# Kernel optimization log

Measured on AMD Instinct MI355X. Metric: run time of the kernel, lower is better.

## Reference

```python
import jax, jax.numpy as jnp
import numpy as np

B, P, M, C = 128, 8732, 16, 3
THRESHOLD, NEG_POS_RATIO, ALPHA = 0.5, 3, 1.0


def xy_to_cxcy(xy):
    return jnp.concatenate([(xy[..., 2:] + xy[..., :2]) / 2.0, xy[..., 2:] - xy[..., :2]], axis=-1)


def cxcy_to_xy(cxcy):
    return jnp.concatenate([cxcy[..., :2] - cxcy[..., 2:] / 2.0, cxcy[..., :2] + cxcy[..., 2:] / 2.0], axis=-1)


def cxcy_to_gcxgcy(cxcy, priors_cxcy):
    return jnp.concatenate([
        (cxcy[..., :2] - priors_cxcy[..., :2]) / (priors_cxcy[..., 2:] / 10.0),
        jnp.log(cxcy[..., 2:] / priors_cxcy[..., 2:]) * 5.0], axis=-1)


def jaccard(a, b):
    # a: (M,4) xyxy, b: (P,4) xyxy -> (M,P) IoU
    lt = jnp.maximum(a[:, None, :2], b[None, :, :2])
    rb = jnp.minimum(a[:, None, 2:], b[None, :, 2:])
    wh = jnp.clip(rb - lt, 0.0)
    inter = wh[..., 0] * wh[..., 1]
    area_a = (a[:, 2] - a[:, 0]) * (a[:, 3] - a[:, 1])
    area_b = (b[:, 2] - b[:, 0]) * (b[:, 3] - b[:, 1])
    return inter / (area_a[:, None] + area_b[None, :] - inter)


def setup_inputs() -> dict:
    key = jax.random.key(0)
    k1, k2, k3, k4, k5, k6 = jax.random.split(key, 6)
    predicted_locs = jax.random.normal(k1, (B, P, 4), dtype=jnp.float32)
    predicted_scores = jax.random.normal(k2, (B, P, C), dtype=jnp.float32)
    xy = jax.random.uniform(k3, (B, M, 2), minval=0.0, maxval=0.7)
    wh = jax.random.uniform(k4, (B, M, 2), minval=0.05, maxval=0.3)
    boxes = jnp.concatenate([xy, xy + wh], axis=-1).astype(jnp.float32)
    labels = jax.random.randint(k5, (B, M), 1, 4)  # classes {1,2,3}
    pc = jax.random.uniform(k6, (P, 2), minval=0.0, maxval=1.0)
    pwh = jax.random.uniform(jax.random.fold_in(k6, 1), (P, 2), minval=0.05, maxval=0.5)
    priors_cxcy = jnp.concatenate([pc, pwh], axis=-1).astype(jnp.float32)
    return {"predicted_locs": predicted_locs, "predicted_scores": predicted_scores,
            "boxes": boxes, "labels": labels, "priors_cxcy": priors_cxcy}


def _match_one(boxes_i, labels_i, priors_xy, priors_cxcy):
    ov = jaccard(boxes_i, priors_xy)                # (M, P)
    ov_prior = ov.max(axis=0)                       # best overlap per prior
    obj_prior = ov.argmax(axis=0)                   # best object per prior
    prior_obj = ov.argmax(axis=1)                   # best prior per object
    n_obj = boxes_i.shape[0]
    obj_prior = obj_prior.at[prior_obj].set(jnp.arange(n_obj))
    ov_prior = ov_prior.at[prior_obj].set(1.0)
    lab = jnp.where(ov_prior < THRESHOLD, 0, labels_i[obj_prior])
    tl = cxcy_to_gcxgcy(xy_to_cxcy(boxes_i[obj_prior]), priors_cxcy)
    return tl, lab


def reference(predicted_locs, predicted_scores, boxes, labels, priors_cxcy):
    priors_xy = cxcy_to_xy(priors_cxcy)
    true_locs, true_classes = jax.vmap(_match_one, in_axes=(0, 0, None, None))(
        boxes, labels, priors_xy, priors_cxcy)      # (B,P,4), (B,P)
    positive = true_classes > 0                      # (B,P)
    n_pos = positive.sum(axis=1)                     # (B,)
    n_pos_total = n_pos.sum()

    # localization loss: L1Loss (mean over selected positive elements)
    l1 = jnp.abs(predicted_locs - true_locs).sum(axis=-1)   # (B,P)
    loc_loss = jnp.where(n_pos_total > 0,
                         (l1 * positive).sum() / (4.0 * jnp.maximum(n_pos_total, 1).astype(jnp.float32)),
                         0.0)

    # multi-label one-hot targets (classes 1,2,3; 3 = pair -> targets cols 1&2)
    tc = true_classes.reshape(-1)
    ignore = tc == -1
    pair = tc == 3
    target = jax.nn.one_hot(tc + 1, 5, dtype=predicted_scores.dtype)[:, 1:4]  # (B*P,3)
    target = target.at[:, 1].set(jnp.where(pair, 1.0, target[:, 1]))
    target = target.at[:, 2].set(jnp.where(pair, 1.0, target[:, 2]))

    # BCEWithLogits, summed over classes
    logits = predicted_scores.reshape(-1, C)
    bce = (jnp.logaddexp(0.0, logits) - logits * target).sum(axis=1)  # (B*P,)
    conf_all = jnp.where(ignore, 0.0, bce).reshape(true_classes.shape)  # (B,P)

    conf_pos = (conf_all * positive).sum()
    conf_neg = jnp.where(positive, 0.0, conf_all)
    conf_neg_sorted = -jnp.sort(-conf_neg, axis=1)   # descending per row
    ranks = jnp.arange(P)[None, :]
    hard_neg = ranks < (NEG_POS_RATIO * n_pos)[:, None]
    conf_hard_neg = (conf_neg_sorted * hard_neg).sum()

    conf_loss = (conf_hard_neg + conf_pos) / (1e-10 + n_pos_total.astype(jnp.float32))
    total = conf_loss + ALPHA * loc_loss
    return total, conf_loss, loc_loss, n_pos
```

## Files before the change

kernel.cpp:

```cpp
#include <hip/hip_runtime.h>
#include <hip/hip_fp16.h>
#include <cstdint>
#include <cmath>

#define B_ 128
#define P_ 8732
#define QU_ 2183
#define M_ 16
#define NT 1024
#define NW 16
#define NP9 9

__device__ __forceinline__ float softplusf(float x) {
    float e = __builtin_amdgcn_exp2f(fabsf(x) * -1.44269504f);
    return fmaxf(x, 0.0f) + 0.69314718f * __builtin_amdgcn_logf(1.0f + e);
}

__device__ __forceinline__ float wred_sum_f(float v) {
#pragma unroll
    for (int o = 32; o > 0; o >>= 1) v += __shfl_down(v, o, 64);
    return v;
}
__device__ __forceinline__ int wred_sum_i(int v) {
#pragma unroll
    for (int o = 32; o > 0; o >>= 1) v += __shfl_down(v, o, 64);
    return v;
}

__global__ __launch_bounds__(NT) void mbox_match_kernel(
    const float* __restrict__ plocs,
    const float* __restrict__ pscores,
    const float* __restrict__ boxes,
    const int*   __restrict__ labels,
    const float* __restrict__ priors,
    unsigned char* __restrict__ objov,
    unsigned short* __restrict__ bcew,
    int2* __restrict__ cand,
    float* __restrict__ pcf, float* __restrict__ plc, int* __restrict__ pnp,
    unsigned int* __restrict__ gz)
{
    __shared__ unsigned long long s_ovp[QU_];
    __shared__ float s_boxes[M_ * 4];
    __shared__ float s_area[M_];
    __shared__ int   s_labels[M_];
    __shared__ float s_pf[2 * NW];
    __shared__ int   s_pi[NW];

    const int bk = blockIdx.x;
    const int r  = bk >> 2;
    const int q  = bk & 3;
    const int tid = threadIdx.x;
    const int lane = tid & 63;
    const int wid = tid >> 6;

    if (bk == 0 && tid < 4) gz[tid] = 0u;

    if (tid < M_ * 4) s_boxes[tid] = boxes[r * M_ * 4 + tid];
    if (tid >= 64 && tid < 64 + M_) s_labels[tid - 64] = labels[r * M_ + (tid - 64)];
    for (int i = tid; i < QU_; i += NT) s_ovp[i] = 15ull;
    __syncthreads();
    if (tid < M_) {
        float x0 = s_boxes[tid*4+0], y0 = s_boxes[tid*4+1];
        float x1 = s_boxes[tid*4+2], y1 = s_boxes[tid*4+3];
        s_area[tid] = (x1 - x0) * (y1 - y0);
    }
    __syncthreads();

    const int p0 = q * QU_;

    {
        const int m = wid;
        const float bx0 = s_boxes[m*4+0], by0 = s_boxes[m*4+1];
        const float bx1 = s_boxes[m*4+2], by1 = s_boxes[m*4+3];
        const float marea = s_area[m];
        const unsigned long long tag = (unsigned long long)(15 - m);
        float bv = -1.0f; int bi = 0x7FFFFFFF;
        for (int p = p0 + lane; p < p0 + QU_; p += 64) {
            float4 pr = ((const float4*)priors)[p];
            float px0 = pr.x - pr.z * 0.5f;
            float py0 = pr.y - pr.w * 0.5f;
            float px1 = pr.x + pr.z * 0.5f;
            float py1 = pr.y + pr.w * 0.5f;
            float ltx = fmaxf(bx0, px0);
            float lty = fmaxf(by0, py0);
            float rbx = fminf(bx1, px1);
            float rby = fminf(by1, py1);
            float wx = fmaxf(rbx - ltx, 0.0f);
            float wy = fmaxf(rby - lty, 0.0f);
            float inter = wx * wy;
            float ov = inter * __builtin_amdgcn_rcpf(marea + pr.z * pr.w - inter);
            if (ov > 0.0f) {
                unsigned long long pk =
                    ((unsigned long long)__float_as_uint(ov) << 4) | tag;
                atomicMax(&s_ovp[p - p0], pk);
            }
            if (ov > bv) { bv = ov; bi = p; }
        }
#pragma unroll
        for (int o = 32; o > 0; o >>= 1) {
            float v2 = __shfl_down(bv, o, 64);
            int   i2 = __shfl_down(bi, o, 64);
            if (v2 > bv || (v2 == bv && i2 < bi)) { bv = v2; bi = i2; }
        }
        if (lane == 0) cand[bk * M_ + m] = make_int2(__float_as_int(bv), bi);
    }
    __syncthreads();

    int np = 0; float cp = 0.0f, ls = 0.0f;
    for (int p = p0 + tid; p < p0 + QU_; p += NT) {
        unsigned long long u = s_ovp[p - p0];
        int   besti = 15 - (int)(u & 15ull);
        float bestv = __uint_as_float((unsigned int)(u >> 4));
        bool pos = bestv >= 0.5f;
        objov[(size_t)r * P_ + p] = (unsigned char)(besti | (pos ? 0x80 : 0));

        const float* sc = pscores + ((size_t)r * P_ + p) * 3;
        float x0 = sc[0], x1 = sc[1], x2 = sc[2];
        int lab = pos ? s_labels[besti] : 0;
        float t0 = (lab == 0) ? 1.0f : 0.0f;
        float t1 = (lab == 1 || lab == 3) ? 1.0f : 0.0f;
        float t2 = (lab == 2 || lab == 3) ? 1.0f : 0.0f;
        float bce = (softplusf(x0) - x0*t0) + (softplusf(x1) - x1*t1) + (softplusf(x2) - x2*t2);
        float hb = 0.0f;
        if (pos) {
            np++; cp += bce;
            float4 pr = ((const float4*)priors)[p];
            float bx0 = s_boxes[besti*4+0], by0 = s_boxes[besti*4+1];
            float bx1 = s_boxes[besti*4+2], by1 = s_boxes[besti*4+3];
            float cx = (bx0 + bx1) * 0.5f, cy = (by0 + by1) * 0.5f;
            float w = bx1 - bx0, hh = by1 - by0;
            float g0 = (cx - pr.x) / (pr.z * 0.1f);
            float g1 = (cy - pr.y) / (pr.w * 0.1f);
            float g2 = logf(w / pr.z) * 5.0f;
            float g3 = logf(hh / pr.w) * 5.0f;
            float4 pl = ((const float4*)plocs)[(size_t)r * P_ + p];
            ls += fabsf(pl.x - g0) + fabsf(pl.y - g1) + fabsf(pl.z - g2) + fabsf(pl.w - g3);
        } else {
            hb = bce;
        }
        bcew[(size_t)r * P_ + p] = __half_as_ushort(__float2half(hb));
    }

    {
        float cpr = wred_sum_f(cp);
        float lsr = wred_sum_f(ls);
        int   npr = wred_sum_i(np);
        if (lane == 0) { s_pf[wid] = cpr; s_pf[NW + wid] = lsr; s_pi[wid] = npr; }
    }
    __syncthreads();
    if (tid == 0) {
        float c2 = 0.0f, l2 = 0.0f; int n2 = 0;
#pragma unroll
        for (int w = 0; w < NW; ++w) { c2 += s_pf[w]; l2 += s_pf[NW + w]; n2 += s_pi[w]; }
        pcf[bk] = c2; plc[bk] = l2; pnp[bk] = n2;
    }
}

__global__ __launch_bounds__(NT) void mbox_loss_kernel(
    const float* __restrict__ plocs,
    const float* __restrict__ pscores,
    const float* __restrict__ boxes,
    const int*   __restrict__ labels,
    const float* __restrict__ priors,
    const unsigned char* __restrict__ objov,
    const unsigned short* __restrict__ bcew,
    const int2* __restrict__ cand,
    const float* __restrict__ pcf, const float* __restrict__ plc,
    const int* __restrict__ pnp,
    float* __restrict__ out,
    unsigned int* __restrict__ g_cnt,
    float* __restrict__ g_conf, float* __restrict__ g_loc, int* __restrict__ g_np)
{
    __shared__ float s_boxes[M_ * 4];
    __shared__ int   s_labels[M_];
    __shared__ int   s_po[M_];
    __shared__ float s_pf[2 * NW];
    __shared__ int   s_pi[NW];
    __shared__ int   s_cnt2[2][NW];
    __shared__ float s_scal[2];
    __shared__ int   s_npos;

    const int r = blockIdx.x;
    const int tid = threadIdx.x;
    const int lane = tid & 63;
    const int wid = tid >> 6;

    if (tid < M_ * 4) s_boxes[tid] = boxes[r * M_ * 4 + tid];
    if (tid >= 64 && tid < 64 + M_) s_labels[tid - 64] = labels[r * M_ + (tid - 64)];
    if (tid >= 128 && tid < 128 + M_) {
        int m = tid - 128;
        int2 c = cand[(r * 4) * M_ + m];
        float v = __int_as_float(c.x); int idx = c.y;
#pragma unroll
        for (int qq = 1; qq < 4; ++qq) {
            int2 c2 = cand[(r * 4 + qq) * M_ + m];
            float v2 = __int_as_float(c2.x);
            if (v2 > v) { v = v2; idx = c2.y; }
        }
        s_po[m] = idx;
    }
    __syncthreads();

    int fv_b[NP9];
#pragma unroll
    for (int i = 0; i < NP9; ++i) {
        int p = tid + i * NT;
        fv_b[i] = (p < P_) ? (int)bcew[(size_t)r * P_ + p] : 0;
    }

    if (wid == 0) {
        float dcp = 0.0f, dls = 0.0f; int dnp = 0;
        if (lane < M_) {
            const int m = lane;
            const int idx = s_po[m];
            bool owner = true;
            for (int m2 = m + 1; m2 < M_; ++m2)
                if (s_po[m2] == idx) owner = false;
            if (owner) {
                unsigned char byte = objov[(size_t)r * P_ + idx];
                bool oldpos = (byte & 0x80) != 0;
                int  oldobj = byte & 15;
                const float* sc = pscores + ((size_t)r * P_ + idx) * 3;
                float x0 = sc[0], x1 = sc[1], x2 = sc[2];
                float S = softplusf(x0) + softplusf(x1) + softplusf(x2);
                float4 pr = ((const float4*)priors)[idx];
                float4 pl = ((const float4*)plocs)[(size_t)r * P_ + idx];
                {
                    int lab = s_labels[m];
                    float t0 = (lab == 0) ? 1.0f : 0.0f;
                    float t1 = (lab == 1 || lab == 3) ? 1.0f : 0.0f;
                    float t2 = (lab == 2 || lab == 3) ? 1.0f : 0.0f;
                    dcp += S - (x0*t0 + x1*t1 + x2*t2);
                    float bx0 = s_boxes[m*4+0], by0 = s_boxes[m*4+1];
                    float bx1 = s_boxes[m*4+2], by1 = s_boxes[m*4+3];
                    float cx = (bx0+bx1)*0.5f, cy = (by0+by1)*0.5f;
                    float w = bx1-bx0, hh = by1-by0;
                    float g0 = (cx - pr.x) / (pr.z * 0.1f);
                    float g1 = (cy - pr.y) / (pr.w * 0.1f);
                    float g2 = logf(w / pr.z) * 5.0f;
                    float g3 = logf(hh / pr.w) * 5.0f;
                    dls += fabsf(pl.x-g0)+fabsf(pl.y-g1)+fabsf(pl.z-g2)+fabsf(pl.w-g3);
                    dnp += 1;
                }
                if (oldpos) {
                    int lab = s_labels[oldobj];
                    float t0 = (lab == 0) ? 1.0f : 0.0f;
                    float t1 = (lab == 1 || lab == 3) ? 1.0f : 0.0f;
                    float t2 = (lab == 2 || lab == 3) ? 1.0f : 0.0f;
                    dcp -= S - (x0*t0 + x1*t1 + x2*t2);
                    float bx0 = s_boxes[oldobj*4+0], by0 = s_boxes[oldobj*4+1];
                    float bx1 = s_boxes[oldobj*4+2], by1 = s_boxes[oldobj*4+3];
                    float cx = (bx0+bx1)*0.5f, cy = (by0+by1)*0.5f;
                    float w = bx1-bx0, hh = by1-by0;
                    float g0 = (cx - pr.x) / (pr.z * 0.1f);
                    float g1 = (cy - pr.y) / (pr.w * 0.1f);
                    float g2 = logf(w / pr.z) * 5.0f;
                    float g3 = logf(hh / pr.w) * 5.0f;
                    dls -= fabsf(pl.x-g0)+fabsf(pl.y-g1)+fabsf(pl.z-g2)+fabsf(pl.w-g3);
                    dnp -= 1;
                }
            }
        }
        dcp = wred_sum_f(dcp);
        dls = wred_sum_f(dls);
        dnp = wred_sum_i(dnp);
        if (lane == 0) {
            float cp = dcp, lsx = dls; int np = dnp;
#pragma unroll
            for (int qq = 0; qq < 4; ++qq) {
                cp  += pcf[r * 4 + qq];
                lsx += plc[r * 4 + qq];
                np  += pnp[r * 4 + qq];
            }
            s_scal[0] = cp; s_scal[1] = lsx; s_npos = np;
        }
    }
    __syncthreads();
    const int npos_row = s_npos;

#pragma unroll
    for (int i = 0; i < NP9; ++i) {
        int p = tid + i * NT;
#pragma unroll
        for (int j = 0; j < M_; ++j)
            if (s_po[j] == p) fv_b[i] = 0;
    }

    int k = 3 * npos_row;
    if (k > P_) k = P_;
    float hard_sum = 0.0f;
    if (k > 0) {
        int lo = -1, hi = 0x7C00;
        for (int it = 0; it < 15; ++it) {
            int mid = (lo + hi) >> 1;
            int c = 0;
#pragma unroll
            for (int i = 0; i < NP9; ++i) c += (fv_b[i] > mid) ? 1 : 0;
            c = wred_sum_i(c);
            if (lane == 0) s_cnt2[it & 1][wid] = c;
            __syncthreads();
            int cnt = 0;
#pragma unroll
            for (int w = 0; w < NW; ++w) cnt += s_cnt2[it & 1][w];
            if (cnt < k) hi = mid; else lo = mid;
        }
        int tb = hi;
        float tval = __half2float(__ushort_as_half((unsigned short)tb));
        float lsum = 0.0f; int lcnt = 0;
#pragma unroll
        for (int i = 0; i < NP9; ++i) {
            if (fv_b[i] > tb) {
                lsum += __half2float(__ushort_as_half((unsigned short)fv_b[i]));
                lcnt++;
            }
        }
        lsum = wred_sum_f(lsum);
        lcnt = wred_sum_i(lcnt);
        if (lane == 0) { s_pf[wid] = lsum; s_pi[wid] = lcnt; }
        __syncthreads();
        if (tid == 0) {
            float sv = 0.0f; int sc2 = 0;
#pragma unroll
            for (int w = 0; w < NW; ++w) { sv += s_pf[w]; sc2 += s_pi[w]; }
            hard_sum = sv + (float)(k - sc2) * tval;
        }
    }

    if (tid == 0) {
        float conf_row = s_scal[0] + hard_sum;
        float loc_row  = s_scal[1];
        out[3 + r] = (float)npos_row;
        atomicAdd(g_conf, conf_row);
        atomicAdd(g_loc,  loc_row);
        atomicAdd(g_np,   npos_row);
        __threadfence();
        unsigned int done = atomicAdd(g_cnt, 1u);
        if (done == B_ - 1) {
            float ct = atomicAdd(g_conf, 0.0f);
            float lt = atomicAdd(g_loc,  0.0f);
            int   np = atomicAdd(g_np,   0);
            float npt = (float)np;
            float conf_loss = ct / (1e-10f + npt);
            float loc_loss = (np > 0) ? lt / (4.0f * fmaxf(npt, 1.0f)) : 0.0f;
            out[0] = conf_loss + loc_loss;
            out[1] = conf_loss;
            out[2] = loc_loss;
        }
    }
}

extern "C" void kernel_launch(void* const* d_in, const int* in_sizes, int n_in,
                              void* d_out, int out_size, void* d_ws, size_t ws_size,
                              hipStream_t stream) {
    const float* plocs   = (const float*)d_in[0];
    const float* pscores = (const float*)d_in[1];
    const float* boxes   = (const float*)d_in[2];
    const int*   labels  = (const int*)  d_in[3];
    const float* priors  = (const float*)d_in[4];
    float* out = (float*)d_out;

    char* ws = (char*)d_ws;
    unsigned int* g_cnt  = (unsigned int*)ws;
    float*        g_conf = (float*)(ws + 4);
    float*        g_loc  = (float*)(ws + 8);
    int*          g_np   = (int*)(ws + 12);
    float*        pcf    = (float*)(ws + 64);
    float*        plc    = (float*)(ws + 2112);
    int*          pnp    = (int*)(ws + 4160);
    int2*         cand   = (int2*)(ws + 8192);
    unsigned char* objov = (unsigned char*)(ws + 73728);
    unsigned short* bcew = (unsigned short*)(ws + 73728 + (size_t)B_ * P_);

    mbox_match_kernel<<<4 * B_, NT, 0, stream>>>(plocs, pscores, boxes, labels, priors,
                                                 objov, bcew, cand, pcf, plc, pnp,
                                                 (unsigned int*)ws);
    mbox_loss_kernel<<<B_, NT, 0, stream>>>(plocs, pscores, boxes, labels, priors,
                                            objov, bcew, cand, pcf, plc, pnp,
                                            out, g_cnt, g_conf, g_loc, g_np);
}
```

Before: 120.6 us.

## Fuse match and loss kernels using per-row last-block completion counter

Merges the two launches into one kernel. Each of the four quarter-row blocks bumps a per-row atomic counter, and the last block to finish runs the hard-negative selection and final reduction. The per-row BCE values are staged in shared memory, reusing the overlap buffer, instead of registers. Positive priors are zeroed with a direct scatter rather than a 16-way compare per element. This removes a launch gap and the global synchronisation between stages, but adds a memset, fence overhead, and a serial tail that runs on only one block per row.

```diff
diff --git a/kernel.cpp b/kernel.cpp
--- a/kernel.cpp
+++ b/kernel.cpp
@@ -27,7 +27,7 @@
     return v;
 }
 
-__global__ __launch_bounds__(NT) void mbox_match_kernel(
+__global__ __launch_bounds__(NT) void mbox_fused_kernel(
     const float* __restrict__ plocs,
     const float* __restrict__ pscores,
     const float* __restrict__ boxes,
@@ -37,7 +37,10 @@
     unsigned short* __restrict__ bcew,
     int2* __restrict__ cand,
     float* __restrict__ pcf, float* __restrict__ plc, int* __restrict__ pnp,
-    unsigned int* __restrict__ gz)
+    unsigned int* __restrict__ row_cnt,
+    float* __restrict__ out,
+    unsigned int* __restrict__ g_cnt,
+    float* __restrict__ g_conf, float* __restrict__ g_loc, int* __restrict__ g_np)
 {
     __shared__ unsigned long long s_ovp[QU_];
     __shared__ float s_boxes[M_ * 4];
@@ -45,6 +48,13 @@
     __shared__ int   s_labels[M_];
     __shared__ float s_pf[2 * NW];
     __shared__ int   s_pi[NW];
+    __shared__ int   s_po[M_];
+    __shared__ int   s_cnt2[2][NW];
+    __shared__ float s_scal[2];
+    __shared__ int   s_npos;
+    __shared__ int   s_islast;
+
+    unsigned short* s_fv = (unsigned short*)s_ovp;
 
     const int bk = blockIdx.x;
     const int r  = bk >> 2;
@@ -52,8 +62,6 @@
     const int tid = threadIdx.x;
     const int lane = tid & 63;
     const int wid = tid >> 6;
-
-    if (bk == 0 && tid < 4) gz[tid] = 0u;
 
     if (tid < M_ * 4) s_boxes[tid] = boxes[r * M_ * 4 + tid];
     if (tid >= 64 && tid < 64 + M_) s_labels[tid - 64] = labels[r * M_ + (tid - 64)];
@@ -153,60 +161,36 @@
 #pragma unroll
         for (int w = 0; w < NW; ++w) { c2 += s_pf[w]; l2 += s_pf[NW + w]; n2 += s_pi[w]; }
         pcf[bk] = c2; plc[bk] = l2; pnp[bk] = n2;
-    }
-}
-
-__global__ __launch_bounds__(NT) void mbox_loss_kernel(
-    const float* __restrict__ plocs,
-    const float* __restrict__ pscores,
-    const float* __restrict__ boxes,
-    const int*   __restrict__ labels,
-    const float* __restrict__ priors,
-    const unsigned char* __restrict__ objov,
-    const unsigned short* __restrict__ bcew,
-    const int2* __restrict__ cand,
-    const float* __restrict__ pcf, const float* __restrict__ plc,
-    const int* __restrict__ pnp,
-    float* __restrict__ out,
-    unsigned int* __restrict__ g_cnt,
-    float* __restrict__ g_conf, float* __restrict__ g_loc, int* __restrict__ g_np)
-{
-    __shared__ float s_boxes[M_ * 4];
-    __shared__ int   s_labels[M_];
-    __shared__ int   s_po[M_];
-    __shared__ float s_pf[2 * NW];
-    __shared__ int   s_pi[NW];
-    __shared__ int   s_cnt2[2][NW];
-    __shared__ float s_scal[2];
-    __shared__ int   s_npos;
-
-    const int r = blockIdx.x;
-    const int tid = threadIdx.x;
-    const int lane = tid & 63;
-    const int wid = tid >> 6;
-
-    if (tid < M_ * 4) s_boxes[tid] = boxes[r * M_ * 4 + tid];
-    if (tid >= 64 && tid < 64 + M_) s_labels[tid - 64] = labels[r * M_ + (tid - 64)];
-    if (tid >= 128 && tid < 128 + M_) {
-        int m = tid - 128;
-        int2 c = cand[(r * 4) * M_ + m];
+        __builtin_amdgcn_fence(__ATOMIC_RELEASE, "agent");
+        unsigned int prev = atomicAdd(&row_cnt[r], 1u);
+        if (prev == 3u) {
+            __builtin_amdgcn_fence(__ATOMIC_ACQUIRE, "agent");
+            s_islast = 1;
+        } else {
+            s_islast = 0;
+        }
+    }
+    __syncthreads();
+    if (!s_islast) return;
+
+
+    if (tid < M_) {
+        int2 c = cand[(r * 4) * M_ + tid];
         float v = __int_as_float(c.x); int idx = c.y;
 #pragma unroll
         for (int qq = 1; qq < 4; ++qq) {
-            int2 c2 = cand[(r * 4 + qq) * M_ + m];
+            int2 c2 = cand[(r * 4 + qq) * M_ + tid];
             float v2 = __int_as_float(c2.x);
             if (v2 > v) { v = v2; idx = c2.y; }
         }
-        s_po[m] = idx;
-    }
-    __syncthreads();
-
-    int fv_b[NP9];
+        s_po[tid] = idx;
+    }
 #pragma unroll
     for (int i = 0; i < NP9; ++i) {
         int p = tid + i * NT;
-        fv_b[i] = (p < P_) ? (int)bcew[(size_t)r * P_ + p] : 0;
-    }
+        if (p < P_) s_fv[p] = bcew[(size_t)r * P_ + p];
+    }
+    __syncthreads();
 
     if (wid == 0) {
         float dcp = 0.0f, dls = 0.0f; int dnp = 0;
@@ -265,26 +249,19 @@
         dls = wred_sum_f(dls);
         dnp = wred_sum_i(dnp);
         if (lane == 0) {
-            float cp = dcp, lsx = dls; int np = dnp;
+            float cp2 = dcp, lsx = dls; int np2 = dnp;
 #pragma unroll
             for (int qq = 0; qq < 4; ++qq) {
-                cp  += pcf[r * 4 + qq];
+                cp2 += pcf[r * 4 + qq];
                 lsx += plc[r * 4 + qq];
-                np  += pnp[r * 4 + qq];
-            }
-            s_scal[0] = cp; s_scal[1] = lsx; s_npos = np;
-        }
-    }
+                np2 += pnp[r * 4 + qq];
+            }
+            s_scal[0] = cp2; s_scal[1] = lsx; s_npos = np2;
+        }
+    }
+    if (wid == 1 && lane < M_) s_fv[s_po[lane]] = 0;
     __syncthreads();
     const int npos_row = s_npos;
-
-#pragma unroll
-    for (int i = 0; i < NP9; ++i) {
-        int p = tid + i * NT;
-#pragma unroll
-        for (int j = 0; j < M_; ++j)
-            if (s_po[j] == p) fv_b[i] = 0;
-    }
 
     int k = 3 * npos_row;
     if (k > P_) k = P_;
@@ -295,7 +272,10 @@
             int mid = (lo + hi) >> 1;
             int c = 0;
 #pragma unroll
-            for (int i = 0; i < NP9; ++i) c += (fv_b[i] > mid) ? 1 : 0;
+            for (int i = 0; i < NP9; ++i) {
+                int p = tid + i * NT;
+                if (p < P_) c += ((int)s_fv[p] > mid) ? 1 : 0;
+            }
             c = wred_sum_i(c);
             if (lane == 0) s_cnt2[it & 1][wid] = c;
             __syncthreads();
@@ -309,9 +289,13 @@
         float lsum = 0.0f; int lcnt = 0;
 #pragma unroll
         for (int i = 0; i < NP9; ++i) {
-            if (fv_b[i] > tb) {
-                lsum += __half2float(__ushort_as_half((unsigned short)fv_b[i]));
-                lcnt++;
+            int p = tid + i * NT;
+            if (p < P_) {
+                int fv = (int)s_fv[p];
+                if (fv > tb) {
+                    lsum += __half2float(__ushort_as_half((unsigned short)fv));
+                    lcnt++;
+                }
             }
         }
         lsum = wred_sum_f(lsum);
@@ -338,10 +322,10 @@
         if (done == B_ - 1) {
             float ct = atomicAdd(g_conf, 0.0f);
             float lt = atomicAdd(g_loc,  0.0f);
-            int   np = atomicAdd(g_np,   0);
-            float npt = (float)np;
+            int   np2 = atomicAdd(g_np,   0);
+            float npt = (float)np2;
             float conf_loss = ct / (1e-10f + npt);
-            float loc_loss = (np > 0) ? lt / (4.0f * fmaxf(npt, 1.0f)) : 0.0f;
+            float loc_loss = (np2 > 0) ? lt / (4.0f * fmaxf(npt, 1.0f)) : 0.0f;
             out[0] = conf_loss + loc_loss;
             out[1] = conf_loss;
             out[2] = loc_loss;
@@ -360,21 +344,22 @@
     float* out = (float*)d_out;
 
     char* ws = (char*)d_ws;
-    unsigned int* g_cnt  = (unsigned int*)ws;
-    float*        g_conf = (float*)(ws + 4);
-    float*        g_loc  = (float*)(ws + 8);
-    int*          g_np   = (int*)(ws + 12);
-    float*        pcf    = (float*)(ws + 64);
-    float*        plc    = (float*)(ws + 2112);
-    int*          pnp    = (int*)(ws + 4160);
-    int2*         cand   = (int2*)(ws + 8192);
-    unsigned char* objov = (unsigned char*)(ws + 73728);
-    unsigned short* bcew = (unsigned short*)(ws + 73728 + (size_t)B_ * P_);
-
-    mbox_match_kernel<<<4 * B_, NT, 0, stream>>>(plocs, pscores, boxes, labels, priors,
-                                                 objov, bcew, cand, pcf, plc, pnp,
-                                                 (unsigned int*)ws);
-    mbox_loss_kernel<<<B_, NT, 0, stream>>>(plocs, pscores, boxes, labels, priors,
-                                            objov, bcew, cand, pcf, plc, pnp,
-                                            out, g_cnt, g_conf, g_loc, g_np);
-}
+    unsigned int* g_cnt   = (unsigned int*)ws;
+    float*        g_conf  = (float*)(ws + 4);
+    float*        g_loc   = (float*)(ws + 8);
+    int*          g_np    = (int*)(ws + 12);
+    unsigned int* row_cnt = (unsigned int*)(ws + 16);
+    float*        pcf     = (float*)(ws + 576);
+    float*        plc     = (float*)(ws + 2624);
+    int*          pnp     = (int*)(ws + 4672);
+    int2*         cand    = (int2*)(ws + 8192);
+    unsigned char* objov  = (unsigned char*)(ws + 73728);
+    unsigned short* bcew  = (unsigned short*)(ws + 73728 + (size_t)B_ * P_);
+
+    hipMemsetAsync(ws, 0, 528, stream);
+
+    mbox_fused_kernel<<<4 * B_, NT, 0, stream>>>(
+        plocs, pscores, boxes, labels, priors,
+        objov, bcew, cand, pcf, plc, pnp, row_cnt,
+        out, g_cnt, g_conf, g_loc, g_np);
+}
```

New measurement: 134.2 us. +11.3%, slower.

## Assign priors to threads and loop over objects, dropping shared-memory atomic max

Applied to the files above, without the earlier changes.

The match kernel now gives each thread up to three priors and loops over all 16 boxes in registers, in place of one wavefront per box doing 64-bit atomicMax into a shared per-prior array. Best object per prior is kept in registers. Best prior per object is found with a wave shuffle reduction per box, then a cross-wave reduction in shared memory. Prior and score loads are issued at kernel start so they overlap the box setup. Tie-breaking on equal overlaps follows the in-register max rather than the packed atomic tag, so the index chosen may differ from before.

```diff
diff --git a/kernel.cpp b/kernel.cpp
--- a/kernel.cpp
+++ b/kernel.cpp
@@ -10,6 +10,7 @@
 #define NT 1024
 #define NW 16
 #define NP9 9
+#define TAIL_ (QU_ - 2*NT)
 
 __device__ __forceinline__ float softplusf(float x) {
     float e = __builtin_amdgcn_exp2f(fabsf(x) * -1.44269504f);
@@ -25,6 +26,39 @@
 #pragma unroll
     for (int o = 32; o > 0; o >>= 1) v += __shfl_down(v, o, 64);
     return v;
+}
+
+__device__ __forceinline__ void phaseD(
+    int r, int p, float bv, int bm, float4 pr,
+    float x0, float x1, float x2,
+    const float* s_boxes, const int* s_labels,
+    const float* __restrict__ plocs,
+    unsigned char* __restrict__ objov, unsigned short* __restrict__ bcew,
+    int& np, float& cp, float& ls)
+{
+    bool pos = bv >= 0.5f;
+    objov[(size_t)r * P_ + p] = (unsigned char)(bm | (pos ? 0x80 : 0));
+    int lab = pos ? s_labels[bm] : 0;
+    float t0 = (lab == 0) ? 1.0f : 0.0f;
+    float t1 = (lab == 1 || lab == 3) ? 1.0f : 0.0f;
+    float t2 = (lab == 2 || lab == 3) ? 1.0f : 0.0f;
+    float bce = (softplusf(x0) - x0*t0) + (softplusf(x1) - x1*t1) + (softplusf(x2) - x2*t2);
+    float hb = 0.0f;
+    if (pos) {
+        np++; cp += bce;
+        float4 bb = ((const float4*)s_boxes)[bm];
+        float cx = (bb.x + bb.z) * 0.5f, cy = (bb.y + bb.w) * 0.5f;
+        float w = bb.z - bb.x, hh = bb.w - bb.y;
+        float g0 = (cx - pr.x) / (pr.z * 0.1f);
+        float g1 = (cy - pr.y) / (pr.w * 0.1f);
+        float g2 = logf(w / pr.z) * 5.0f;
+        float g3 = logf(hh / pr.w) * 5.0f;
+        float4 pl = ((const float4*)plocs)[(size_t)r * P_ + p];
+        ls += fabsf(pl.x - g0) + fabsf(pl.y - g1) + fabsf(pl.z - g2) + fabsf(pl.w - g3);
+    } else {
+        hb = bce;
+    }
+    bcew[(size_t)r * P_ + p] = __half_as_ushort(__float2half(hb));
 }
 
 __global__ __launch_bounds__(NT) void mbox_match_kernel(
@@ -39,10 +73,10 @@
     float* __restrict__ pcf, float* __restrict__ plc, int* __restrict__ pnp,
     unsigned int* __restrict__ gz)
 {
-    __shared__ unsigned long long s_ovp[QU_];
     __shared__ float s_boxes[M_ * 4];
     __shared__ float s_area[M_];
     __shared__ int   s_labels[M_];
+    __shared__ int2  s_cand[NW][M_];
     __shared__ float s_pf[2 * NW];
     __shared__ int   s_pi[NW];
 
@@ -52,12 +86,28 @@
     const int tid = threadIdx.x;
     const int lane = tid & 63;
     const int wid = tid >> 6;
+    const int p0 = q * QU_;
 
     if (bk == 0 && tid < 4) gz[tid] = 0u;
+
+    const int  pA = p0 + tid;
+    const int  pB = p0 + NT + tid;
+    const bool cok = tid < TAIL_;
+    const int  pC = cok ? (p0 + 2 * NT + tid) : pA;
+
+    float4 prA = ((const float4*)priors)[pA];
+    float4 prB = ((const float4*)priors)[pB];
+    float4 prC = ((const float4*)priors)[pC];
+
+    const float* scA = pscores + ((size_t)r * P_ + pA) * 3;
+    const float* scB = pscores + ((size_t)r * P_ + pB) * 3;
+    const float* scC = pscores + ((size_t)r * P_ + pC) * 3;
+    float xA0 = scA[0], xA1 = scA[1], xA2 = scA[2];
+    float xB0 = scB[0], xB1 = scB[1], xB2 = scB[2];
+    float xC0 = scC[0], xC1 = scC[1], xC2 = scC[2];
 
     if (tid < M_ * 4) s_boxes[tid] = boxes[r * M_ * 4 + tid];
     if (tid >= 64 && tid < 64 + M_) s_labels[tid - 64] = labels[r * M_ + (tid - 64)];
-    for (int i = tid; i < QU_; i += NT) s_ovp[i] = 15ull;
     __syncthreads();
     if (tid < M_) {
         float x0 = s_boxes[tid*4+0], y0 = s_boxes[tid*4+1];
@@ -66,88 +116,89 @@
     }
     __syncthreads();
 
-    const int p0 = q * QU_;
-
-    {
-        const int m = wid;
-        const float bx0 = s_boxes[m*4+0], by0 = s_boxes[m*4+1];
-        const float bx1 = s_boxes[m*4+2], by1 = s_boxes[m*4+3];
-        const float marea = s_area[m];
-        const unsigned long long tag = (unsigned long long)(15 - m);
-        float bv = -1.0f; int bi = 0x7FFFFFFF;
-        for (int p = p0 + lane; p < p0 + QU_; p += 64) {
-            float4 pr = ((const float4*)priors)[p];
-            float px0 = pr.x - pr.z * 0.5f;
-            float py0 = pr.y - pr.w * 0.5f;
-            float px1 = pr.x + pr.z * 0.5f;
-            float py1 = pr.y + pr.w * 0.5f;
-            float ltx = fmaxf(bx0, px0);
-            float lty = fmaxf(by0, py0);
-            float rbx = fminf(bx1, px1);
-            float rby = fminf(by1, py1);
-            float wx = fmaxf(rbx - ltx, 0.0f);
-            float wy = fmaxf(rby - lty, 0.0f);
-            float inter = wx * wy;
-            float ov = inter * __builtin_amdgcn_rcpf(marea + pr.z * pr.w - inter);
-            if (ov > 0.0f) {
-                unsigned long long pk =
-                    ((unsigned long long)__float_as_uint(ov) << 4) | tag;
-                atomicMax(&s_ovp[p - p0], pk);
-            }
-            if (ov > bv) { bv = ov; bi = p; }
-        }
+    float aX0 = prA.x - prA.z*0.5f, aY0 = prA.y - prA.w*0.5f;
+    float aX1 = prA.x + prA.z*0.5f, aY1 = prA.y + prA.w*0.5f;
+    float aAr = prA.z * prA.w;
+    float bX0 = prB.x - prB.z*0.5f, bY0 = prB.y - prB.w*0.5f;
+    float bX1 = prB.x + prB.z*0.5f, bY1 = prB.y + prB.w*0.5f;
+    float bAr = prB.z * prB.w;
+    float cX0 = prC.x - prC.z*0.5f, cY0 = prC.y - prC.w*0.5f;
+    float cX1 = prC.x + prC.z*0.5f, cY1 = prC.y + prC.w*0.5f;
+    float cAr = prC.z * prC.w;
+
+    float bvA = -1.0f, bvB = -1.0f, bvC = -1.0f;
+    int   bmA = 0,     bmB = 0,     bmC = 0;
+
+#pragma unroll
+    for (int m = 0; m < M_; ++m) {
+        float4 bb = ((const float4*)s_boxes)[m];
+        float mar = s_area[m];
+
+        float ltx, lty, rbx, rby, wx, wy, inter;
+
+        ltx = fmaxf(bb.x, aX0); lty = fmaxf(bb.y, aY0);
+        rbx = fminf(bb.z, aX1); rby = fminf(bb.w, aY1);
+        wx = fmaxf(rbx - ltx, 0.0f); wy = fmaxf(rby - lty, 0.0f);
+        inter = wx * wy;
+        float ovA = inter * __builtin_amdgcn_rcpf(mar + aAr - inter);
+
+        ltx = fmaxf(bb.x, bX0); lty = fmaxf(bb.y, bY0);
+        rbx = fminf(bb.z, bX1); rby = fminf(bb.w, bY1);
+        wx = fmaxf(rbx - ltx, 0.0f); wy = fmaxf(rby - lty, 0.0f);
+        inter = wx * wy;
+        float ovB = inter * __builtin_amdgcn_rcpf(mar + bAr - inter);
+
+        ltx = fmaxf(bb.x, cX0); lty = fmaxf(bb.y, cY0);
+        rbx = fminf(bb.z, cX1); rby = fminf(bb.w, cY1);
+        wx = fmaxf(rbx - ltx, 0.0f); wy = fmaxf(rby - lty, 0.0f);
+        inter = wx * wy;
+        float ovC = inter * __builtin_amdgcn_rcpf(mar + cAr - inter);
+        ovC = cok ? ovC : -1.0f;
+
+        if (ovA > bvA) { bvA = ovA; bmA = m; }
+        if (ovB > bvB) { bvB = ovB; bmB = m; }
+        if (ovC > bvC) { bvC = ovC; bmC = m; }
+
+        float v = ovA; int which = 0;
+        if (ovB > v) { v = ovB; which = 1; }
+        if (ovC > v) { v = ovC; which = 2; }
+        int idx = p0 + tid + (which << 10);
+
 #pragma unroll
         for (int o = 32; o > 0; o >>= 1) {
-            float v2 = __shfl_down(bv, o, 64);
-            int   i2 = __shfl_down(bi, o, 64);
-            if (v2 > bv || (v2 == bv && i2 < bi)) { bv = v2; bi = i2; }
-        }
-        if (lane == 0) cand[bk * M_ + m] = make_int2(__float_as_int(bv), bi);
-    }
+            float v2 = __shfl_down(v, o, 64);
+            int   i2 = __shfl_down(idx, o, 64);
+            if (v2 > v || (v2 == v && i2 < idx)) { v = v2; idx = i2; }
+        }
+        if (lane == 0) s_cand[wid][m] = make_int2(__float_as_int(v), idx);
+    }
+
+    int np = 0; float cp = 0.0f, ls = 0.0f;
+    phaseD(r, pA, bvA, bmA, prA, xA0, xA1, xA2, s_boxes, s_labels,
+           plocs, objov, bcew, np, cp, ls);
+    phaseD(r, pB, bvB, bmB, prB, xB0, xB1, xB2, s_boxes, s_labels,
+           plocs, objov, bcew, np, cp, ls);
+    if (cok)
+        phaseD(r, pC, bvC, bmC, prC, xC0, xC1, xC2, s_boxes, s_labels,
+               plocs, objov, bcew, np, cp, ls);
+
+    cp = wred_sum_f(cp);
+    ls = wred_sum_f(ls);
+    np = wred_sum_i(np);
+    if (lane == 0) { s_pf[wid] = cp; s_pf[NW + wid] = ls; s_pi[wid] = np; }
     __syncthreads();
 
-    int np = 0; float cp = 0.0f, ls = 0.0f;
-    for (int p = p0 + tid; p < p0 + QU_; p += NT) {
-        unsigned long long u = s_ovp[p - p0];
-        int   besti = 15 - (int)(u & 15ull);
-        float bestv = __uint_as_float((unsigned int)(u >> 4));
-        bool pos = bestv >= 0.5f;
-        objov[(size_t)r * P_ + p] = (unsigned char)(besti | (pos ? 0x80 : 0));
-
-        const float* sc = pscores + ((size_t)r * P_ + p) * 3;
-        float x0 = sc[0], x1 = sc[1], x2 = sc[2];
-        int lab = pos ? s_labels[besti] : 0;
-        float t0 = (lab == 0) ? 1.0f : 0.0f;
-        float t1 = (lab == 1 || lab == 3) ? 1.0f : 0.0f;
-        float t2 = (lab == 2 || lab == 3) ? 1.0f : 0.0f;
-        float bce = (softplusf(x0) - x0*t0) + (softplusf(x1) - x1*t1) + (softplusf(x2) - x2*t2);
-        float hb = 0.0f;
-        if (pos) {
-            np++; cp += bce;
-            float4 pr = ((const float4*)priors)[p];
-            float bx0 = s_boxes[besti*4+0], by0 = s_boxes[besti*4+1];
-            float bx1 = s_boxes[besti*4+2], by1 = s_boxes[besti*4+3];
-            float cx = (bx0 + bx1) * 0.5f, cy = (by0 + by1) * 0.5f;
-            float w = bx1 - bx0, hh = by1 - by0;
-            float g0 = (cx - pr.x) / (pr.z * 0.1f);
-            float g1 = (cy - pr.y) / (pr.w * 0.1f);
-            float g2 = logf(w / pr.z) * 5.0f;
-            float g3 = logf(hh / pr.w) * 5.0f;
-            float4 pl = ((const float4*)plocs)[(size_t)r * P_ + p];
-            ls += fabsf(pl.x - g0) + fabsf(pl.y - g1) + fabsf(pl.z - g2) + fabsf(pl.w - g3);
-        } else {
-            hb = bce;
-        }
-        bcew[(size_t)r * P_ + p] = __half_as_ushort(__float2half(hb));
-    }
-
-    {
-        float cpr = wred_sum_f(cp);
-        float lsr = wred_sum_f(ls);
-        int   npr = wred_sum_i(np);
-        if (lane == 0) { s_pf[wid] = cpr; s_pf[NW + wid] = lsr; s_pi[wid] = npr; }
-    }
-    __syncthreads();
+    if (tid < M_) {
+        int2 c0 = s_cand[0][tid];
+        float bv = __int_as_float(c0.x); int bidx = c0.y;
+#pragma unroll
+        for (int w = 1; w < NW; ++w) {
+            int2 c = s_cand[w][tid];
+            float v = __int_as_float(c.x);
+            if (v > bv || (v == bv && c.y < bidx)) { bv = v; bidx = c.y; }
+        }
+        cand[bk * M_ + tid] = make_int2(__float_as_int(bv), bidx);
+    }
     if (tid == 0) {
         float c2 = 0.0f, l2 = 0.0f; int n2 = 0;
 #pragma unroll
```

Result: slower. 136.8 us (+13.4%).
